# Optimization experiments

Hardware: AMD Instinct MI355X
Metric: run time of the kernel (lower is better)

The kernel has to match this reference:

```python
import jax, jax.numpy as jnp
import numpy as np

NEG_SLOPE = 0.2


def gat_conv(x, edge_index, W, a_src, a_dst, b):
    # PyG GATConv (heads=1, add_self_loops=True, concat -> out_channels)
    N = x.shape[0]
    h = x @ W                                   # [N, F_out]
    loops = jnp.arange(N, dtype=edge_index.dtype)
    src = jnp.concatenate([edge_index[0], loops])   # message sources (x_j)
    dst = jnp.concatenate([edge_index[1], loops])   # message targets (x_i)
    # attention logits: e = LeakyReLU(a_src . h_j + a_dst . h_i)
    alpha_s = h @ a_src                          # [N]
    alpha_d = h @ a_dst                          # [N]
    e = jax.nn.leaky_relu(alpha_s[src] + alpha_d[dst], NEG_SLOPE)  # [E+N]
    # segment softmax over incoming edges of each dst node
    m = jax.ops.segment_max(e, dst, num_segments=N)
    e = jnp.exp(e - m[dst])
    denom = jax.ops.segment_sum(e, dst, num_segments=N)
    alpha = e / denom[dst]                       # self-loops guarantee denom > 0
    # weighted scatter-sum aggregation
    out = jax.ops.segment_sum(alpha[:, None] * h[src], dst, num_segments=N)
    return out + b


def setup_inputs() -> dict:
    key = jax.random.key(0)
    ks = jax.random.split(key, 10)
    N, E, F_in, H, F_out = 100000, 3200000, 54, 16, 16
    x = jax.random.normal(ks[0], (N, F_in), dtype=jnp.float32)
    edge_index = jax.random.randint(ks[1], (2, E), 0, N, dtype=jnp.int64)
    s1 = 1.0 / np.sqrt(F_in)
    s2 = 1.0 / np.sqrt(H)
    return {
        "x": x,
        "edge_index": edge_index,
        "W1": jax.random.uniform(ks[2], (F_in, H), jnp.float32, -s1, s1),
        "a1_src": jax.random.uniform(ks[3], (H,), jnp.float32, -s2, s2),
        "a1_dst": jax.random.uniform(ks[4], (H,), jnp.float32, -s2, s2),
        "b1": jnp.zeros((H,), jnp.float32),
        "W2": jax.random.uniform(ks[5], (H, F_out), jnp.float32, -s2, s2),
        "a2_src": jax.random.uniform(ks[6], (F_out,), jnp.float32, -0.25, 0.25),
        "a2_dst": jax.random.uniform(ks[7], (F_out,), jnp.float32, -0.25, 0.25),
        "b2": jnp.zeros((F_out,), jnp.float32),
    }


def reference(x, edge_index, W1, a1_src, a1_dst, b1, W2, a2_src, a2_dst, b2):
    h = gat_conv(x, edge_index, W1, a1_src, a1_dst, b1)
    h = jax.nn.elu(h)
    # dropout p=0.5 is identity in eval mode
    out = gat_conv(h, edge_index, W2, a2_src, a2_dst, b2)
    return out
```

## Files before the change

kernel.cpp:

```cpp
#include <hip/hip_runtime.h>
#include <hip/hip_bf16.h>

typedef __hip_bfloat16 bf16;

static constexpr int N_NODES = 100000;
static constexpr int N_EDGES = 3200000;
static constexpr int F_IN    = 54;
static constexpr int F_HID   = 16;

static constexpr int BSHIFT    = 7;
static constexpr int BNODES    = 128;
static constexpr int NBUCK     = (N_NODES + BNODES - 1) / BNODES;
static constexpr int CAP_B     = 5120;
static constexpr int BIN_CHUNK = 8192;
static constexpr int GRDB      = (N_EDGES + BIN_CHUNK - 1) / BIN_CHUNK;
static constexpr int GRDN_F    = (N_NODES + 1023) / 1024;

static constexpr size_t WS_FLAGS  = 0;
static constexpr size_t WS_ADST   = 4;
static constexpr size_t WS_ADST2  = 100004;
static constexpr size_t WS_BCNT   = 200004;
static constexpr size_t WS_ROWBEG = 201028;
static constexpr size_t WS_ROWCNT = 301028;
static constexpr size_t WS_HC1    = 401028;
static constexpr size_t WS_HC2    = 2001028;
static constexpr size_t WS_BEDGES = 3601028;
static constexpr size_t WS_SRCS   = 7604868;
static constexpr size_t WS_BUCKET_END = WS_SRCS + (size_t)NBUCK * CAP_B;
static constexpr size_t WS_FB_DEN     = 3601028;
static constexpr size_t WS_FB_AS      = 3701028;
static constexpr size_t WS_ATOMIC_END = 3801028;

__device__ __forceinline__ float lrelu(float v) { return fmaxf(v, 0.2f * v); }
__device__ __forceinline__ float loadf(const void* p, int i, bool f32) {
    return f32 ? ((const float*)p)[i] : __bfloat162float(((const bf16*)p)[i]);
}
__device__ __forceinline__ unsigned f2bf(float f) {
    unsigned u = __float_as_uint(f);
    return (u + 0x7FFFu + ((u >> 16) & 1u)) >> 16;
}

__global__ __launch_bounds__(256) void k_probe0(
    const void* __restrict__ x, const void* __restrict__ ei,
    int* __restrict__ flags, int* __restrict__ bcnt)
{
    __shared__ int cnt, nz;
    const int t = threadIdx.x;
    if (t == 0) { cnt = 0; nz = 0; }
    __syncthreads();
    const unsigned u = ((const unsigned*)x)[t];
    if ((u & 0x7FFFu) >= 0x4800u) atomicAdd(&cnt, 1);
    if (t < 64) {
        if (((const unsigned*)ei)[2 * t + 1] != 0u) atomicAdd(&nz, 1);
    }
    for (int i = t; i < 1024; i += 256) bcnt[i] = 0;
    __syncthreads();
    if (t == 0) flags[0] = ((cnt >= 16) ? 1 : 0) | ((nz == 0) ? 2 : 0);
}

__global__ __launch_bounds__(1024, 8) void k_binfeat(
    const void* __restrict__ ei, const void* __restrict__ x,
    const void* __restrict__ W1, const void* __restrict__ a_s,
    const void* __restrict__ a_d, const int* __restrict__ flags,
    int* __restrict__ bcnt, int* __restrict__ bedges,
    unsigned* __restrict__ hc, float* __restrict__ adst)
{
    __shared__ int            hist[NBUCK];
    __shared__ int            base[NBUCK];
    __shared__ int            cval[BIN_CHUNK];
    __shared__ unsigned short cbkt[BIN_CHUNK];
    __shared__ float Wl[F_IN * F_HID];
    __shared__ float asl[F_HID];
    __shared__ float adl[F_HID];
    const int t = threadIdx.x;
    const bool f32 = flags[0] & 1;
    const bool i64 = flags[0] & 2;

    if (blockIdx.x < GRDB) {
        const int e0 = blockIdx.x * BIN_CHUNK;
        const int valid = min(BIN_CHUNK, N_EDGES - e0);
        for (int i = t; i < NBUCK; i += 1024) hist[i] = 0;
        __syncthreads();
#pragma unroll
        for (int i = 0; i < BIN_CHUNK / 1024; ++i) {
            const int idx = i * 1024 + t;
            const int e = e0 + idx;
            if (idx < valid) {
                int s, d;
                if (i64) {
                    s = ((const int*)ei)[2 * (size_t)e];
                    d = ((const int*)ei)[2 * ((size_t)N_EDGES + e)];
                } else {
                    s = ((const int*)ei)[e];
                    d = ((const int*)ei)[(size_t)N_EDGES + e];
                }
                const int b = d >> BSHIFT;
                cval[idx] = (s << BSHIFT) | (d & (BNODES - 1));
                cbkt[idx] = (unsigned short)b;
                atomicAdd(&hist[b], 1);
            }
        }
        __syncthreads();
        for (int i = t; i < NBUCK; i += 1024) {
            const int c = hist[i];
            base[i] = c ? atomicAdd(&bcnt[i], c) : 0;
            hist[i] = 0;
        }
        __syncthreads();
#pragma unroll
        for (int i = 0; i < BIN_CHUNK / 1024; ++i) {
            const int idx = i * 1024 + t;
            if (idx < valid) {
                const int b = cbkt[idx];
                const int r = atomicAdd(&hist[b], 1);
                const int pos = base[b] + r;
                if (pos < CAP_B) bedges[(size_t)b * CAP_B + pos] = cval[idx];
            }
        }
    } else {
        for (int i = t; i < F_IN * F_HID; i += 1024) Wl[i] = loadf(W1, i, f32);
        if (t < F_HID) { asl[t] = loadf(a_s, t, f32); adl[t] = loadf(a_d, t, f32); }
        __syncthreads();
        const int node = (blockIdx.x - GRDB) * 1024 + t;
        if (node >= N_NODES) return;

        float h[F_HID];
#pragma unroll
        for (int k = 0; k < F_HID; ++k) h[k] = 0.f;
        if (f32) {
            const float2* xp = (const float2*)((const float*)x + (size_t)node * F_IN);
#pragma unroll
            for (int j = 0; j < F_IN / 2; ++j) {
                const float2 v = xp[j];
#pragma unroll
                for (int k = 0; k < F_HID; ++k) {
                    h[k] = fmaf(v.x, Wl[(2*j)   * F_HID + k], h[k]);
                    h[k] = fmaf(v.y, Wl[(2*j+1) * F_HID + k], h[k]);
                }
            }
        } else {
            const unsigned* xu = (const unsigned*)x + (size_t)node * (F_IN / 2);
#pragma unroll
            for (int j = 0; j < F_IN / 2; ++j) {
                const unsigned u = xu[j];
                const float v0 = __uint_as_float(u << 16);
                const float v1 = __uint_as_float(u & 0xFFFF0000u);
#pragma unroll
                for (int k = 0; k < F_HID; ++k) {
                    h[k] = fmaf(v0, Wl[(2*j)   * F_HID + k], h[k]);
                    h[k] = fmaf(v1, Wl[(2*j+1) * F_HID + k], h[k]);
                }
            }
        }
        float s = 0.f, d = 0.f;
#pragma unroll
        for (int k = 0; k < F_HID; ++k) { s = fmaf(h[k], asl[k], s); d = fmaf(h[k], adl[k], d); }
        adst[node] = d;
        const unsigned ab = f2bf(s) << 16;
        unsigned pk[F_HID];
#pragma unroll
        for (int k = 0; k < F_HID; ++k) pk[k] = f2bf(h[k]) | ab;
        uint4* hb = (uint4*)(hc + (size_t)node * F_HID);
#pragma unroll
        for (int q = 0; q < 4; ++q)
            hb[q] = make_uint4(pk[4*q], pk[4*q+1], pk[4*q+2], pk[4*q+3]);
    }
}

__global__ __launch_bounds__(512) void k_bsort(
    const int* __restrict__ bcnt, const int* __restrict__ bedges,
    int* __restrict__ rowbeg, int* __restrict__ rowcnt, int* __restrict__ srcs)
{
    __shared__ int hist[BNODES];
    __shared__ int scan[BNODES];
    __shared__ int cur[BNODES];
    const int t = threadIdx.x;
    const int b = blockIdx.x;
    const int n0 = b << BSHIFT;
    if (t < BNODES) hist[t] = 0;
    __syncthreads();
    const int cnt = min(bcnt[b], CAP_B);
    const int* be = bedges + (size_t)b * CAP_B;
    for (int e = t; e < cnt; e += 512)
        atomicAdd(&hist[be[e] & (BNODES - 1)], 1);
    __syncthreads();
    if (t < BNODES) scan[t] = (hist[t] + 3) & ~3;
    __syncthreads();
#pragma unroll
    for (int off = 1; off < BNODES; off <<= 1) {
        const int v = (t < BNODES && t >= off) ? scan[t - off] : 0;
        __syncthreads();
        if (t < BNODES) scan[t] += v;
        __syncthreads();
    }
    if (t < BNODES) {
        const int ex = scan[t] - ((hist[t] + 3) & ~3);
        cur[t] = ex;
        const int node = n0 + t;
        if (node < N_NODES) {
            rowbeg[node] = b * CAP_B + ex;
            rowcnt[node] = hist[t];
        }
    }
    __syncthreads();
    for (int e = t; e < cnt; e += 512) {
        const int p = be[e];
        const int dl = p & (BNODES - 1);
        const int r = atomicAdd(&cur[dl], 1);
        if (r < CAP_B) srcs[(size_t)b * CAP_B + r] = p >> BSHIFT;
    }
}

__global__ __launch_bounds__(256) void k_agg1(
    const int* __restrict__ rowbeg, const int* __restrict__ rowcnt,
    const int* __restrict__ srcs, const float* __restrict__ adst,
    const unsigned* __restrict__ hc, const void* __restrict__ b1,
    const void* __restrict__ W2, const void* __restrict__ a_s2,
    const void* __restrict__ a_d2, const int* __restrict__ flags,
    unsigned* __restrict__ hc2, float* __restrict__ adst2)
{
    __shared__ float Wl[F_HID * F_HID];
    __shared__ float asl[F_HID];
    __shared__ float adl[F_HID];
    __shared__ float bl[F_HID];
    const bool f32 = flags[0] & 1;
    const int t = threadIdx.x;
    if (t < F_HID * F_HID) Wl[t] = loadf(W2, t, f32);
    if (t < F_HID) {
        asl[t] = loadf(a_s2, t, f32);
        adl[t] = loadf(a_d2, t, f32);
        bl[t]  = loadf(b1, t, f32);
    }
    __syncthreads();

    const int k = t & 15;
    const int node = blockIdx.x * 16 + (t >> 4);
    const float adn = adst[node];
    const unsigned vs = hc[(size_t)node * F_HID + k];
    const float w0 = __expf(lrelu(__uint_as_float(vs & 0xFFFF0000u) + adn));
    float denom = w0;
    float acc = w0 * __uint_as_float(vs << 16);
    const int n = rowcnt[node];
    const int* sp = srcs + rowbeg[node];
    int i = 0;
    if (n >= 8) {
        int4 sa = *(const int4*)(sp);
        int4 sb = *(const int4*)(sp + 4);
        while (true) {
            const bool more = (i + 16 <= n);
            int4 na, nb;
            if (more) {
                na = *(const int4*)(sp + i + 8);
                nb = *(const int4*)(sp + i + 12);
            }
            const unsigned v0 = hc[(size_t)sa.x * F_HID + k];
            const unsigned v1 = hc[(size_t)sa.y * F_HID + k];
            const unsigned v2 = hc[(size_t)sa.z * F_HID + k];
            const unsigned v3 = hc[(size_t)sa.w * F_HID + k];
            const unsigned v4 = hc[(size_t)sb.x * F_HID + k];
            const unsigned v5 = hc[(size_t)sb.y * F_HID + k];
            const unsigned v6 = hc[(size_t)sb.z * F_HID + k];
            const unsigned v7 = hc[(size_t)sb.w * F_HID + k];
            const float e0 = __expf(lrelu(__uint_as_float(v0 & 0xFFFF0000u) + adn));
            const float e1 = __expf(lrelu(__uint_as_float(v1 & 0xFFFF0000u) + adn));
            const float e2 = __expf(lrelu(__uint_as_float(v2 & 0xFFFF0000u) + adn));
            const float e3 = __expf(lrelu(__uint_as_float(v3 & 0xFFFF0000u) + adn));
            const float e4 = __expf(lrelu(__uint_as_float(v4 & 0xFFFF0000u) + adn));
            const float e5 = __expf(lrelu(__uint_as_float(v5 & 0xFFFF0000u) + adn));
            const float e6 = __expf(lrelu(__uint_as_float(v6 & 0xFFFF0000u) + adn));
            const float e7 = __expf(lrelu(__uint_as_float(v7 & 0xFFFF0000u) + adn));
            denom += (e0 + e1 + e2 + e3) + (e4 + e5 + e6 + e7);
            acc = fmaf(e0, __uint_as_float(v0 << 16), acc);
            acc = fmaf(e1, __uint_as_float(v1 << 16), acc);
            acc = fmaf(e2, __uint_as_float(v2 << 16), acc);
            acc = fmaf(e3, __uint_as_float(v3 << 16), acc);
            acc = fmaf(e4, __uint_as_float(v4 << 16), acc);
            acc = fmaf(e5, __uint_as_float(v5 << 16), acc);
            acc = fmaf(e6, __uint_as_float(v6 << 16), acc);
            acc = fmaf(e7, __uint_as_float(v7 << 16), acc);
            i += 8;
            if (!more) break;
            sa = na; sb = nb;
        }
    }
    if (i + 4 <= n) {
        const int4 sa = *(const int4*)(sp + i);
        const unsigned v0 = hc[(size_t)sa.x * F_HID + k];
        const unsigned v1 = hc[(size_t)sa.y * F_HID + k];
        const unsigned v2 = hc[(size_t)sa.z * F_HID + k];
        const unsigned v3 = hc[(size_t)sa.w * F_HID + k];
        const float e0 = __expf(lrelu(__uint_as_float(v0 & 0xFFFF0000u) + adn));
        const float e1 = __expf(lrelu(__uint_as_float(v1 & 0xFFFF0000u) + adn));
        const float e2 = __expf(lrelu(__uint_as_float(v2 & 0xFFFF0000u) + adn));
        const float e3 = __expf(lrelu(__uint_as_float(v3 & 0xFFFF0000u) + adn));
        denom += (e0 + e1) + (e2 + e3);
        acc = fmaf(e0, __uint_as_float(v0 << 16), acc);
        acc = fmaf(e1, __uint_as_float(v1 << 16), acc);
        acc = fmaf(e2, __uint_as_float(v2 << 16), acc);
        acc = fmaf(e3, __uint_as_float(v3 << 16), acc);
        i += 4;
    }
    for (; i < n; ++i) {
        const unsigned v = hc[(size_t)sp[i] * F_HID + k];
        const float w = __expf(lrelu(__uint_as_float(v & 0xFFFF0000u) + adn));
        denom += w;
        acc = fmaf(w, __uint_as_float(v << 16), acc);
    }
    float z = acc / denom + bl[k];
    z = z > 0.f ? z : expm1f(z);

    float hh = 0.f;
#pragma unroll
    for (int j = 0; j < F_HID; ++j) {
        const float zj = __shfl(z, j, 16);
        hh = fmaf(zj, Wl[j * F_HID + k], hh);
    }
    float s2 = hh * asl[k], d2 = hh * adl[k];
#pragma unroll
    for (int off = 1; off < 16; off <<= 1) {
        s2 += __shfl_xor(s2, off, 16);
        d2 += __shfl_xor(d2, off, 16);
    }
    hc2[(size_t)node * F_HID + k] = f2bf(hh) | (f2bf(s2) << 16);
    if (k == 0) adst2[node] = d2;
}

__global__ __launch_bounds__(256) void k_agg2(
    const int* __restrict__ rowbeg, const int* __restrict__ rowcnt,
    const int* __restrict__ srcs, const float* __restrict__ adst,
    const unsigned* __restrict__ hc, const void* __restrict__ b2,
    const int* __restrict__ flags, float* __restrict__ outp)
{
    const bool f32 = flags[0] & 1;
    const int t = threadIdx.x;
    const int k = t & 15;
    const int node = blockIdx.x * 16 + (t >> 4);
    const float adn = adst[node];
    const unsigned vs = hc[(size_t)node * F_HID + k];
    const float w0 = __expf(lrelu(__uint_as_float(vs & 0xFFFF0000u) + adn));
    float denom = w0;
    float acc = w0 * __uint_as_float(vs << 16);
    const int n = rowcnt[node];
    const int* sp = srcs + rowbeg[node];
    int i = 0;
    if (n >= 8) {
        int4 sa = *(const int4*)(sp);
        int4 sb = *(const int4*)(sp + 4);
        while (true) {
            const bool more = (i + 16 <= n);
            int4 na, nb;
            if (more) {
                na = *(const int4*)(sp + i + 8);
                nb = *(const int4*)(sp + i + 12);
            }
            const unsigned v0 = hc[(size_t)sa.x * F_HID + k];
            const unsigned v1 = hc[(size_t)sa.y * F_HID + k];
            const unsigned v2 = hc[(size_t)sa.z * F_HID + k];
            const unsigned v3 = hc[(size_t)sa.w * F_HID + k];
            const unsigned v4 = hc[(size_t)sb.x * F_HID + k];
            const unsigned v5 = hc[(size_t)sb.y * F_HID + k];
            const unsigned v6 = hc[(size_t)sb.z * F_HID + k];
            const unsigned v7 = hc[(size_t)sb.w * F_HID + k];
            const float e0 = __expf(lrelu(__uint_as_float(v0 & 0xFFFF0000u) + adn));
            const float e1 = __expf(lrelu(__uint_as_float(v1 & 0xFFFF0000u) + adn));
            const float e2 = __expf(lrelu(__uint_as_float(v2 & 0xFFFF0000u) + adn));
            const float e3 = __expf(lrelu(__uint_as_float(v3 & 0xFFFF0000u) + adn));
            const float e4 = __expf(lrelu(__uint_as_float(v4 & 0xFFFF0000u) + adn));
            const float e5 = __expf(lrelu(__uint_as_float(v5 & 0xFFFF0000u) + adn));
            const float e6 = __expf(lrelu(__uint_as_float(v6 & 0xFFFF0000u) + adn));
            const float e7 = __expf(lrelu(__uint_as_float(v7 & 0xFFFF0000u) + adn));
            denom += (e0 + e1 + e2 + e3) + (e4 + e5 + e6 + e7);
            acc = fmaf(e0, __uint_as_float(v0 << 16), acc);
            acc = fmaf(e1, __uint_as_float(v1 << 16), acc);
            acc = fmaf(e2, __uint_as_float(v2 << 16), acc);
            acc = fmaf(e3, __uint_as_float(v3 << 16), acc);
            acc = fmaf(e4, __uint_as_float(v4 << 16), acc);
            acc = fmaf(e5, __uint_as_float(v5 << 16), acc);
            acc = fmaf(e6, __uint_as_float(v6 << 16), acc);
            acc = fmaf(e7, __uint_as_float(v7 << 16), acc);
            i += 8;
            if (!more) break;
            sa = na; sb = nb;
        }
    }
    if (i + 4 <= n) {
        const int4 sa = *(const int4*)(sp + i);
        const unsigned v0 = hc[(size_t)sa.x * F_HID + k];
        const unsigned v1 = hc[(size_t)sa.y * F_HID + k];
        const unsigned v2 = hc[(size_t)sa.z * F_HID + k];
        const unsigned v3 = hc[(size_t)sa.w * F_HID + k];
        const float e0 = __expf(lrelu(__uint_as_float(v0 & 0xFFFF0000u) + adn));
        const float e1 = __expf(lrelu(__uint_as_float(v1 & 0xFFFF0000u) + adn));
        const float e2 = __expf(lrelu(__uint_as_float(v2 & 0xFFFF0000u) + adn));
        const float e3 = __expf(lrelu(__uint_as_float(v3 & 0xFFFF0000u) + adn));
        denom += (e0 + e1) + (e2 + e3);
        acc = fmaf(e0, __uint_as_float(v0 << 16), acc);
        acc = fmaf(e1, __uint_as_float(v1 << 16), acc);
        acc = fmaf(e2, __uint_as_float(v2 << 16), acc);
        acc = fmaf(e3, __uint_as_float(v3 << 16), acc);
        i += 4;
    }
    for (; i < n; ++i) {
        const unsigned v = hc[(size_t)sp[i] * F_HID + k];
        const float w = __expf(lrelu(__uint_as_float(v & 0xFFFF0000u) + adn));
        denom += w;
        acc = fmaf(w, __uint_as_float(v << 16), acc);
    }
    outp[(size_t)node * F_HID + k] = acc / denom + loadf(b2, k, f32);
}

__global__ __launch_bounds__(256) void k_feat1(
    const void* __restrict__ x, const void* __restrict__ W1,
    const void* __restrict__ a_s, const void* __restrict__ a_d,
    const int* __restrict__ flags,
    float* __restrict__ hbuf, float* __restrict__ asrc, float* __restrict__ adst)
{
    const bool f32 = flags[0] & 1;
    __shared__ float Wl[F_IN * F_HID];
    __shared__ float asl[F_HID];
    __shared__ float adl[F_HID];
    const int t = threadIdx.x;
    for (int i = t; i < F_IN * F_HID; i += 256) Wl[i] = loadf(W1, i, f32);
    if (t < F_HID) { asl[t] = loadf(a_s, t, f32); adl[t] = loadf(a_d, t, f32); }
    __syncthreads();
    const int node = blockIdx.x * 256 + t;
    if (node >= N_NODES) return;
    float h[F_HID];
#pragma unroll
    for (int k = 0; k < F_HID; ++k) h[k] = 0.f;
    if (f32) {
        const float2* xp = (const float2*)((const float*)x + (size_t)node * F_IN);
#pragma unroll
        for (int j = 0; j < F_IN / 2; ++j) {
            const float2 v = xp[j];
#pragma unroll
            for (int k = 0; k < F_HID; ++k) {
                h[k] = fmaf(v.x, Wl[(2*j)   * F_HID + k], h[k]);
                h[k] = fmaf(v.y, Wl[(2*j+1) * F_HID + k], h[k]);
            }
        }
    } else {
        const unsigned* xu = (const unsigned*)x + (size_t)node * (F_IN / 2);
#pragma unroll
        for (int j = 0; j < F_IN / 2; ++j) {
            const unsigned u = xu[j];
            const float v0 = __uint_as_float(u << 16);
            const float v1 = __uint_as_float(u & 0xFFFF0000u);
#pragma unroll
            for (int k = 0; k < F_HID; ++k) {
                h[k] = fmaf(v0, Wl[(2*j)   * F_HID + k], h[k]);
                h[k] = fmaf(v1, Wl[(2*j+1) * F_HID + k], h[k]);
            }
        }
    }
    float s = 0.f, d = 0.f;
#pragma unroll
    for (int k = 0; k < F_HID; ++k) { s = fmaf(h[k], asl[k], s); d = fmaf(h[k], adl[k], d); }
    asrc[node] = s; adst[node] = d;
    float4* hb = (float4*)(hbuf + (size_t)node * F_HID);
#pragma unroll
    for (int q = 0; q < 4; ++q)
        hb[q] = make_float4(h[4*q], h[4*q+1], h[4*q+2], h[4*q+3]);
}

__global__ __launch_bounds__(256) void k_selfinit(
    const float* __restrict__ asrc, const float* __restrict__ adst,
    const float* __restrict__ h, float* __restrict__ denom, float* __restrict__ acc)
{
    const int t = blockIdx.x * 256 + threadIdx.x;
    if (t >= N_NODES * F_HID) return;
    const int n = t >> 4;
    const float w0 = __expf(lrelu(asrc[n] + adst[n]));
    if ((t & 15) == 0) denom[n] = w0;
    acc[t] = w0 * h[t];
}

__global__ __launch_bounds__(256) void k_edge(
    const void* __restrict__ ei, const int* __restrict__ flags,
    const float* __restrict__ asrc, const float* __restrict__ adst,
    const float* __restrict__ hbuf,
    float* __restrict__ denom, float* __restrict__ acc)
{
    const int e = blockIdx.x * 256 + threadIdx.x;
    if (e >= N_EDGES) return;
    int s, d;
    if (flags[0] & 2) {
        const long long* e64 = (const long long*)ei;
        s = (int)e64[e]; d = (int)e64[(size_t)N_EDGES + e];
    } else {
        const int* e32 = (const int*)ei;
        s = e32[e]; d = e32[(size_t)N_EDGES + e];
    }
    const float w = __expf(lrelu(asrc[s] + adst[d]));
    atomicAdd(&denom[d], w);
    const float4* hs = (const float4*)(hbuf + (size_t)s * F_HID);
    float* ad = acc + (size_t)d * F_HID;
#pragma unroll
    for (int q = 0; q < 4; ++q) {
        const float4 hv = hs[q];
        atomicAdd(ad + 4*q + 0, w * hv.x);
        atomicAdd(ad + 4*q + 1, w * hv.y);
        atomicAdd(ad + 4*q + 2, w * hv.z);
        atomicAdd(ad + 4*q + 3, w * hv.w);
    }
}

__global__ __launch_bounds__(256) void k_div_elu(
    float* __restrict__ acc, const float* __restrict__ denom,
    const void* __restrict__ b1, const int* __restrict__ flags)
{
    const bool f32 = flags[0] & 1;
    const int t = blockIdx.x * 256 + threadIdx.x;
    if (t >= N_NODES * F_HID) return;
    const float v = acc[t] / denom[t >> 4] + loadf(b1, t & 15, f32);
    acc[t] = v > 0.f ? v : expm1f(v);
}

__global__ __launch_bounds__(256) void k_mid(
    const float* __restrict__ z,
    const void* __restrict__ W2, const void* __restrict__ a_s2,
    const void* __restrict__ a_d2, const int* __restrict__ flags,
    float* __restrict__ h2, float* __restrict__ asrc, float* __restrict__ adst)
{
    const bool f32 = flags[0] & 1;
    __shared__ float Wl[F_HID * F_HID];
    __shared__ float asl[F_HID];
    __shared__ float adl[F_HID];
    const int t = threadIdx.x;
    if (t < F_HID * F_HID) Wl[t] = loadf(W2, t, f32);
    if (t < F_HID) { asl[t] = loadf(a_s2, t, f32); adl[t] = loadf(a_d2, t, f32); }
    __syncthreads();
    const int node = blockIdx.x * 256 + t;
    if (node >= N_NODES) return;
    float zr[F_HID];
    const float4* zi = (const float4*)(z + (size_t)node * F_HID);
#pragma unroll
    for (int q = 0; q < 4; ++q) {
        const float4 zv = zi[q];
        zr[4*q+0]=zv.x; zr[4*q+1]=zv.y; zr[4*q+2]=zv.z; zr[4*q+3]=zv.w;
    }
    float h[F_HID];
#pragma unroll
    for (int k = 0; k < F_HID; ++k) h[k] = 0.f;
#pragma unroll
    for (int j = 0; j < F_HID; ++j) {
        const float zv = zr[j];
#pragma unroll
        for (int k = 0; k < F_HID; ++k) h[k] = fmaf(zv, Wl[j * F_HID + k], h[k]);
    }
    float s = 0.f, d = 0.f;
#pragma unroll
    for (int k = 0; k < F_HID; ++k) { s = fmaf(h[k], asl[k], s); d = fmaf(h[k], adl[k], d); }
    asrc[node] = s; adst[node] = d;
    float4* hb = (float4*)(h2 + (size_t)node * F_HID);
#pragma unroll
    for (int q = 0; q < 4; ++q)
        hb[q] = make_float4(h[4*q], h[4*q+1], h[4*q+2], h[4*q+3]);
}

__global__ __launch_bounds__(256) void k_out(
    const float* __restrict__ acc, const float* __restrict__ denom,
    const void* __restrict__ b2, const int* __restrict__ flags,
    float* __restrict__ out)
{
    const bool f32 = flags[0] & 1;
    const int t = blockIdx.x * 256 + threadIdx.x;
    if (t >= N_NODES * F_HID) return;
    out[t] = acc[t] / denom[t >> 4] + loadf(b2, t & 15, f32);
}

__global__ __launch_bounds__(256) void k_diag(float* __restrict__ out, float v)
{
    const int t = blockIdx.x * 256 + threadIdx.x;
    if (t < N_NODES * F_HID) out[t] = v;
}

extern "C" void kernel_launch(void* const* d_in, const int* in_sizes, int n_in,
                              void* d_out, int out_size, void* d_ws, size_t ws_size,
                              hipStream_t stream) {
    const void* x   = d_in[0];
    const void* ei  = d_in[1];
    const void* W1  = d_in[2];
    const void* a1s = d_in[3];
    const void* a1d = d_in[4];
    const void* b1  = d_in[5];
    const void* W2  = d_in[6];
    const void* a2s = d_in[7];
    const void* a2d = d_in[8];
    const void* b2  = d_in[9];
    float* out = (float*)d_out;

    float* ws = (float*)d_ws;
    int*      flags  = (int*)(ws + WS_FLAGS);
    float*    adst   = ws + WS_ADST;
    float*    adst2  = ws + WS_ADST2;
    int*      bcnt   = (int*)(ws + WS_BCNT);
    int*      rowbeg = (int*)(ws + WS_ROWBEG);
    int*      rowcnt = (int*)(ws + WS_ROWCNT);
    unsigned* hc1    = (unsigned*)(ws + WS_HC1);
    unsigned* hc2    = (unsigned*)(ws + WS_HC2);
    int*      bedges = (int*)(ws + WS_BEDGES);
    int*      srcs   = (int*)(ws + WS_SRCS);

    const dim3 blk(256);
    const dim3 grdN((N_NODES + 255) / 256);
    const dim3 grdE((N_EDGES + 255) / 256);
    const dim3 grdO((N_NODES * F_HID + 255) / 256);
    const dim3 grdBF(GRDB + GRDN_F);
    const dim3 grdS(NBUCK);
    const dim3 grdA(N_NODES / 16);

    if (ws_size >= WS_BUCKET_END * 4) {
        k_probe0 <<<dim3(1), blk, 0, stream>>>(x, ei, flags, bcnt);
        k_binfeat<<<grdBF, dim3(1024), 0, stream>>>(ei, x, W1, a1s, a1d, flags,
                                                    bcnt, bedges, hc1, adst);
        k_bsort  <<<grdS, dim3(512), 0, stream>>>(bcnt, bedges, rowbeg, rowcnt, srcs);
        k_agg1   <<<grdA, blk, 0, stream>>>(rowbeg, rowcnt, srcs, adst, hc1,
                                            b1, W2, a2s, a2d, flags, hc2, adst2);
        k_agg2   <<<grdA, blk, 0, stream>>>(rowbeg, rowcnt, srcs, adst2, hc2,
                                            b2, flags, out);
    } else if (ws_size >= WS_ATOMIC_END * 4) {
        float* fb_h   = ws + WS_HC1;
        float* fb_acc = ws + WS_HC2;
        float* fb_den = ws + WS_FB_DEN;
        float* fb_as  = ws + WS_FB_AS;
        float* fb_ad  = ws + WS_ADST;
        k_probe0 <<<dim3(1), blk, 0, stream>>>(x, ei, flags, bcnt);
        k_feat1  <<<grdN, blk, 0, stream>>>(x, W1, a1s, a1d, flags, fb_h, fb_as, fb_ad);
        k_selfinit<<<grdO, blk, 0, stream>>>(fb_as, fb_ad, fb_h, fb_den, fb_acc);
        k_edge   <<<grdE, blk, 0, stream>>>(ei, flags, fb_as, fb_ad, fb_h, fb_den, fb_acc);
        k_div_elu<<<grdO, blk, 0, stream>>>(fb_acc, fb_den, b1, flags);
        k_mid    <<<grdN, blk, 0, stream>>>(fb_acc, W2, a2s, a2d, flags, fb_h, fb_as, fb_ad);
        k_selfinit<<<grdO, blk, 0, stream>>>(fb_as, fb_ad, fb_h, fb_den, fb_acc);
        k_edge   <<<grdE, blk, 0, stream>>>(ei, flags, fb_as, fb_ad, fb_h, fb_den, fb_acc);
        k_out    <<<grdO, blk, 0, stream>>>(fb_acc, fb_den, b2, flags, out);
    } else {
        k_diag<<<grdO, blk, 0, stream>>>(out, (float)(ws_size >> 10));
    }
}
```

Baseline: 258.2 us.

## Drop per-node CSR sort; aggregate bucketed edges with LDS atomics

Removes the k_bsort kernel that built per-node CSR rows from 128-node buckets. Both aggregation kernels now run one 512-thread block per bucket and stream the unsorted bucket edges directly, accumulating softmax numerators and denominators into shared-memory arrays with atomics. This saves a kernel launch plus the global write and read of the sorted source array. In exchange it adds LDS atomic contention and loses the per-node register accumulation, and the summation order becomes nondeterministic.

After: 880.2 us. +241.0%, slower.

```diff
diff --git a/kernel.cpp b/kernel.cpp
--- a/kernel.cpp
+++ b/kernel.cpp
@@ -167,246 +167,193 @@
     }
 }
 
-__global__ __launch_bounds__(512) void k_bsort(
+__global__ __launch_bounds__(512, 4) void k_agg1(
     const int* __restrict__ bcnt, const int* __restrict__ bedges,
-    int* __restrict__ rowbeg, int* __restrict__ rowcnt, int* __restrict__ srcs)
-{
-    __shared__ int hist[BNODES];
-    __shared__ int scan[BNODES];
-    __shared__ int cur[BNODES];
+    const float* __restrict__ adst, const unsigned* __restrict__ hc,
+    const void* __restrict__ b1, const void* __restrict__ W2,
+    const void* __restrict__ a_s2, const void* __restrict__ a_d2,
+    const int* __restrict__ flags,
+    unsigned* __restrict__ hc2, float* __restrict__ adst2)
+{
+    __shared__ float Wl[F_HID * F_HID];
+    __shared__ float asl[F_HID], adl[F_HID], bl[F_HID];
+    __shared__ float adL[BNODES];
+    __shared__ float accL[BNODES * 17];
+    __shared__ float denL[BNODES];
+    const bool f32 = flags[0] & 1;
     const int t = threadIdx.x;
     const int b = blockIdx.x;
     const int n0 = b << BSHIFT;
-    if (t < BNODES) hist[t] = 0;
-    __syncthreads();
-    const int cnt = min(bcnt[b], CAP_B);
-    const int* be = bedges + (size_t)b * CAP_B;
-    for (int e = t; e < cnt; e += 512)
-        atomicAdd(&hist[be[e] & (BNODES - 1)], 1);
-    __syncthreads();
-    if (t < BNODES) scan[t] = (hist[t] + 3) & ~3;
-    __syncthreads();
-#pragma unroll
-    for (int off = 1; off < BNODES; off <<= 1) {
-        const int v = (t < BNODES && t >= off) ? scan[t - off] : 0;
-        __syncthreads();
-        if (t < BNODES) scan[t] += v;
-        __syncthreads();
-    }
-    if (t < BNODES) {
-        const int ex = scan[t] - ((hist[t] + 3) & ~3);
-        cur[t] = ex;
-        const int node = n0 + t;
-        if (node < N_NODES) {
-            rowbeg[node] = b * CAP_B + ex;
-            rowcnt[node] = hist[t];
-        }
-    }
-    __syncthreads();
-    for (int e = t; e < cnt; e += 512) {
-        const int p = be[e];
-        const int dl = p & (BNODES - 1);
-        const int r = atomicAdd(&cur[dl], 1);
-        if (r < CAP_B) srcs[(size_t)b * CAP_B + r] = p >> BSHIFT;
-    }
-}
-
-__global__ __launch_bounds__(256) void k_agg1(
-    const int* __restrict__ rowbeg, const int* __restrict__ rowcnt,
-    const int* __restrict__ srcs, const float* __restrict__ adst,
-    const unsigned* __restrict__ hc, const void* __restrict__ b1,
-    const void* __restrict__ W2, const void* __restrict__ a_s2,
-    const void* __restrict__ a_d2, const int* __restrict__ flags,
-    unsigned* __restrict__ hc2, float* __restrict__ adst2)
-{
-    __shared__ float Wl[F_HID * F_HID];
-    __shared__ float asl[F_HID];
-    __shared__ float adl[F_HID];
-    __shared__ float bl[F_HID];
-    const bool f32 = flags[0] & 1;
-    const int t = threadIdx.x;
     if (t < F_HID * F_HID) Wl[t] = loadf(W2, t, f32);
     if (t < F_HID) {
         asl[t] = loadf(a_s2, t, f32);
         adl[t] = loadf(a_d2, t, f32);
         bl[t]  = loadf(b1, t, f32);
     }
-    __syncthreads();
-
-    const int k = t & 15;
-    const int node = blockIdx.x * 16 + (t >> 4);
-    const float adn = adst[node];
-    const unsigned vs = hc[(size_t)node * F_HID + k];
-    const float w0 = __expf(lrelu(__uint_as_float(vs & 0xFFFF0000u) + adn));
-    float denom = w0;
-    float acc = w0 * __uint_as_float(vs << 16);
-    const int n = rowcnt[node];
-    const int* sp = srcs + rowbeg[node];
-    int i = 0;
-    if (n >= 8) {
-        int4 sa = *(const int4*)(sp);
-        int4 sb = *(const int4*)(sp + 4);
-        while (true) {
-            const bool more = (i + 16 <= n);
-            int4 na, nb;
-            if (more) {
-                na = *(const int4*)(sp + i + 8);
-                nb = *(const int4*)(sp + i + 12);
-            }
-            const unsigned v0 = hc[(size_t)sa.x * F_HID + k];
-            const unsigned v1 = hc[(size_t)sa.y * F_HID + k];
-            const unsigned v2 = hc[(size_t)sa.z * F_HID + k];
-            const unsigned v3 = hc[(size_t)sa.w * F_HID + k];
-            const unsigned v4 = hc[(size_t)sb.x * F_HID + k];
-            const unsigned v5 = hc[(size_t)sb.y * F_HID + k];
-            const unsigned v6 = hc[(size_t)sb.z * F_HID + k];
-            const unsigned v7 = hc[(size_t)sb.w * F_HID + k];
-            const float e0 = __expf(lrelu(__uint_as_float(v0 & 0xFFFF0000u) + adn));
-            const float e1 = __expf(lrelu(__uint_as_float(v1 & 0xFFFF0000u) + adn));
-            const float e2 = __expf(lrelu(__uint_as_float(v2 & 0xFFFF0000u) + adn));
-            const float e3 = __expf(lrelu(__uint_as_float(v3 & 0xFFFF0000u) + adn));
-            const float e4 = __expf(lrelu(__uint_as_float(v4 & 0xFFFF0000u) + adn));
-            const float e5 = __expf(lrelu(__uint_as_float(v5 & 0xFFFF0000u) + adn));
-            const float e6 = __expf(lrelu(__uint_as_float(v6 & 0xFFFF0000u) + adn));
-            const float e7 = __expf(lrelu(__uint_as_float(v7 & 0xFFFF0000u) + adn));
-            denom += (e0 + e1 + e2 + e3) + (e4 + e5 + e6 + e7);
-            acc = fmaf(e0, __uint_as_float(v0 << 16), acc);
-            acc = fmaf(e1, __uint_as_float(v1 << 16), acc);
-            acc = fmaf(e2, __uint_as_float(v2 << 16), acc);
-            acc = fmaf(e3, __uint_as_float(v3 << 16), acc);
-            acc = fmaf(e4, __uint_as_float(v4 << 16), acc);
-            acc = fmaf(e5, __uint_as_float(v5 << 16), acc);
-            acc = fmaf(e6, __uint_as_float(v6 << 16), acc);
-            acc = fmaf(e7, __uint_as_float(v7 << 16), acc);
-            i += 8;
-            if (!more) break;
-            sa = na; sb = nb;
-        }
-    }
-    if (i + 4 <= n) {
-        const int4 sa = *(const int4*)(sp + i);
-        const unsigned v0 = hc[(size_t)sa.x * F_HID + k];
-        const unsigned v1 = hc[(size_t)sa.y * F_HID + k];
-        const unsigned v2 = hc[(size_t)sa.z * F_HID + k];
-        const unsigned v3 = hc[(size_t)sa.w * F_HID + k];
-        const float e0 = __expf(lrelu(__uint_as_float(v0 & 0xFFFF0000u) + adn));
-        const float e1 = __expf(lrelu(__uint_as_float(v1 & 0xFFFF0000u) + adn));
-        const float e2 = __expf(lrelu(__uint_as_float(v2 & 0xFFFF0000u) + adn));
-        const float e3 = __expf(lrelu(__uint_as_float(v3 & 0xFFFF0000u) + adn));
-        denom += (e0 + e1) + (e2 + e3);
-        acc = fmaf(e0, __uint_as_float(v0 << 16), acc);
-        acc = fmaf(e1, __uint_as_float(v1 << 16), acc);
-        acc = fmaf(e2, __uint_as_float(v2 << 16), acc);
-        acc = fmaf(e3, __uint_as_float(v3 << 16), acc);
-        i += 4;
-    }
-    for (; i < n; ++i) {
-        const unsigned v = hc[(size_t)sp[i] * F_HID + k];
-        const float w = __expf(lrelu(__uint_as_float(v & 0xFFFF0000u) + adn));
-        denom += w;
-        acc = fmaf(w, __uint_as_float(v << 16), acc);
-    }
-    float z = acc / denom + bl[k];
-    z = z > 0.f ? z : expm1f(z);
-
-    float hh = 0.f;
-#pragma unroll
-    for (int j = 0; j < F_HID; ++j) {
-        const float zj = __shfl(z, j, 16);
-        hh = fmaf(zj, Wl[j * F_HID + k], hh);
-    }
-    float s2 = hh * asl[k], d2 = hh * adl[k];
-#pragma unroll
-    for (int off = 1; off < 16; off <<= 1) {
-        s2 += __shfl_xor(s2, off, 16);
-        d2 += __shfl_xor(d2, off, 16);
-    }
-    hc2[(size_t)node * F_HID + k] = f2bf(hh) | (f2bf(s2) << 16);
-    if (k == 0) adst2[node] = d2;
-}
-
-__global__ __launch_bounds__(256) void k_agg2(
-    const int* __restrict__ rowbeg, const int* __restrict__ rowcnt,
-    const int* __restrict__ srcs, const float* __restrict__ adst,
-    const unsigned* __restrict__ hc, const void* __restrict__ b2,
-    const int* __restrict__ flags, float* __restrict__ outp)
-{
+    if (t < BNODES) {
+        const int node = n0 + t;
+        adL[t] = (node < N_NODES) ? adst[node] : 0.f;
+    }
+    __syncthreads();
+
+    const int k    = t & 15;
+    const int slot = t >> 4;
+#pragma unroll
+    for (int it = 0; it < 4; ++it) {
+        const int dl = it * 32 + slot;
+        const int node = n0 + dl;
+        if (node < N_NODES) {
+            const unsigned vs = hc[((size_t)node << 4) + k];
+            const float w0 = __expf(lrelu(__uint_as_float(vs & 0xFFFF0000u) + adL[dl]));
+            accL[dl * 17 + k] = w0 * __uint_as_float(vs << 16);
+            if (k == 0) denL[dl] = w0;
+        } else {
+            accL[dl * 17 + k] = 0.f;
+            if (k == 0) denL[dl] = 1.f;
+        }
+    }
+    __syncthreads();
+
+    const int cnt = min(bcnt[b], CAP_B);
+    const int* cv = bedges + (size_t)b * CAP_B;
+    int e = slot;
+    for (; e + 96 < cnt; e += 128) {
+        const int p0 = cv[e], p1 = cv[e + 32], p2 = cv[e + 64], p3 = cv[e + 96];
+        const int d0 = p0 & 127, d1 = p1 & 127, d2 = p2 & 127, d3 = p3 & 127;
+        const unsigned v0 = hc[((size_t)(p0 >> 7) << 4) + k];
+        const unsigned v1 = hc[((size_t)(p1 >> 7) << 4) + k];
+        const unsigned v2 = hc[((size_t)(p2 >> 7) << 4) + k];
+        const unsigned v3 = hc[((size_t)(p3 >> 7) << 4) + k];
+        const float w0 = __expf(lrelu(__uint_as_float(v0 & 0xFFFF0000u) + adL[d0]));
+        const float w1 = __expf(lrelu(__uint_as_float(v1 & 0xFFFF0000u) + adL[d1]));
+        const float w2 = __expf(lrelu(__uint_as_float(v2 & 0xFFFF0000u) + adL[d2]));
+        const float w3 = __expf(lrelu(__uint_as_float(v3 & 0xFFFF0000u) + adL[d3]));
+        atomicAdd(&accL[d0 * 17 + k], w0 * __uint_as_float(v0 << 16));
+        atomicAdd(&accL[d1 * 17 + k], w1 * __uint_as_float(v1 << 16));
+        atomicAdd(&accL[d2 * 17 + k], w2 * __uint_as_float(v2 << 16));
+        atomicAdd(&accL[d3 * 17 + k], w3 * __uint_as_float(v3 << 16));
+        if (k == 0) {
+            atomicAdd(&denL[d0], w0);
+            atomicAdd(&denL[d1], w1);
+            atomicAdd(&denL[d2], w2);
+            atomicAdd(&denL[d3], w3);
+        }
+    }
+    for (; e < cnt; e += 32) {
+        const int p = cv[e];
+        const int dl = p & 127;
+        const unsigned v = hc[((size_t)(p >> 7) << 4) + k];
+        const float w = __expf(lrelu(__uint_as_float(v & 0xFFFF0000u) + adL[dl]));
+        atomicAdd(&accL[dl * 17 + k], w * __uint_as_float(v << 16));
+        if (k == 0) atomicAdd(&denL[dl], w);
+    }
+    __syncthreads();
+
+#pragma unroll
+    for (int it = 0; it < 4; ++it) {
+        const int dl = it * 32 + slot;
+        const int node = n0 + dl;
+        if (node >= N_NODES) continue;
+        float z = accL[dl * 17 + k] / denL[dl] + bl[k];
+        z = z > 0.f ? z : expm1f(z);
+        float hh = 0.f;
+#pragma unroll
+        for (int j = 0; j < F_HID; ++j) {
+            const float zj = __shfl(z, j, 16);
+            hh = fmaf(zj, Wl[j * F_HID + k], hh);
+        }
+        float s2 = hh * asl[k], d2v = hh * adl[k];
+#pragma unroll
+        for (int off = 1; off < 16; off <<= 1) {
+            s2  += __shfl_xor(s2, off, 16);
+            d2v += __shfl_xor(d2v, off, 16);
+        }
+        hc2[((size_t)node << 4) + k] = f2bf(hh) | (f2bf(s2) << 16);
+        if (k == 0) adst2[node] = d2v;
+    }
+}
+
+__global__ __launch_bounds__(512, 4) void k_agg2(
+    const int* __restrict__ bcnt, const int* __restrict__ bedges,
+    const float* __restrict__ adst, const unsigned* __restrict__ hc,
+    const void* __restrict__ b2, const int* __restrict__ flags,
+    float* __restrict__ outp)
+{
+    __shared__ float bl[F_HID];
+    __shared__ float adL[BNODES];
+    __shared__ float accL[BNODES * 17];
+    __shared__ float denL[BNODES];
     const bool f32 = flags[0] & 1;
     const int t = threadIdx.x;
-    const int k = t & 15;
-    const int node = blockIdx.x * 16 + (t >> 4);
-    const float adn = adst[node];
-    const unsigned vs = hc[(size_t)node * F_HID + k];
-    const float w0 = __expf(lrelu(__uint_as_float(vs & 0xFFFF0000u) + adn));
-    float denom = w0;
-    float acc = w0 * __uint_as_float(vs << 16);
-    const int n = rowcnt[node];
-    const int* sp = srcs + rowbeg[node];
-    int i = 0;
-    if (n >= 8) {
-        int4 sa = *(const int4*)(sp);
-        int4 sb = *(const int4*)(sp + 4);
-        while (true) {
-            const bool more = (i + 16 <= n);
-            int4 na, nb;
-            if (more) {
-                na = *(const int4*)(sp + i + 8);
-                nb = *(const int4*)(sp + i + 12);
-            }
-            const unsigned v0 = hc[(size_t)sa.x * F_HID + k];
-            const unsigned v1 = hc[(size_t)sa.y * F_HID + k];
-            const unsigned v2 = hc[(size_t)sa.z * F_HID + k];
-            const unsigned v3 = hc[(size_t)sa.w * F_HID + k];
-            const unsigned v4 = hc[(size_t)sb.x * F_HID + k];
-            const unsigned v5 = hc[(size_t)sb.y * F_HID + k];
-            const unsigned v6 = hc[(size_t)sb.z * F_HID + k];
-            const unsigned v7 = hc[(size_t)sb.w * F_HID + k];
-            const float e0 = __expf(lrelu(__uint_as_float(v0 & 0xFFFF0000u) + adn));
-            const float e1 = __expf(lrelu(__uint_as_float(v1 & 0xFFFF0000u) + adn));
-            const float e2 = __expf(lrelu(__uint_as_float(v2 & 0xFFFF0000u) + adn));
-            const float e3 = __expf(lrelu(__uint_as_float(v3 & 0xFFFF0000u) + adn));
-            const float e4 = __expf(lrelu(__uint_as_float(v4 & 0xFFFF0000u) + adn));
-            const float e5 = __expf(lrelu(__uint_as_float(v5 & 0xFFFF0000u) + adn));
-            const float e6 = __expf(lrelu(__uint_as_float(v6 & 0xFFFF0000u) + adn));
-            const float e7 = __expf(lrelu(__uint_as_float(v7 & 0xFFFF0000u) + adn));
-            denom += (e0 + e1 + e2 + e3) + (e4 + e5 + e6 + e7);
-            acc = fmaf(e0, __uint_as_float(v0 << 16), acc);
-            acc = fmaf(e1, __uint_as_float(v1 << 16), acc);
-            acc = fmaf(e2, __uint_as_float(v2 << 16), acc);
-            acc = fmaf(e3, __uint_as_float(v3 << 16), acc);
-            acc = fmaf(e4, __uint_as_float(v4 << 16), acc);
-            acc = fmaf(e5, __uint_as_float(v5 << 16), acc);
-            acc = fmaf(e6, __uint_as_float(v6 << 16), acc);
-            acc = fmaf(e7, __uint_as_float(v7 << 16), acc);
-            i += 8;
-            if (!more) break;
-            sa = na; sb = nb;
-        }
-    }
-    if (i + 4 <= n) {
-        const int4 sa = *(const int4*)(sp + i);
-        const unsigned v0 = hc[(size_t)sa.x * F_HID + k];
-        const unsigned v1 = hc[(size_t)sa.y * F_HID + k];
-        const unsigned v2 = hc[(size_t)sa.z * F_HID + k];
-        const unsigned v3 = hc[(size_t)sa.w * F_HID + k];
-        const float e0 = __expf(lrelu(__uint_as_float(v0 & 0xFFFF0000u) + adn));
-        const float e1 = __expf(lrelu(__uint_as_float(v1 & 0xFFFF0000u) + adn));
-        const float e2 = __expf(lrelu(__uint_as_float(v2 & 0xFFFF0000u) + adn));
-        const float e3 = __expf(lrelu(__uint_as_float(v3 & 0xFFFF0000u) + adn));
-        denom += (e0 + e1) + (e2 + e3);
-        acc = fmaf(e0, __uint_as_float(v0 << 16), acc);
-        acc = fmaf(e1, __uint_as_float(v1 << 16), acc);
-        acc = fmaf(e2, __uint_as_float(v2 << 16), acc);
-        acc = fmaf(e3, __uint_as_float(v3 << 16), acc);
-        i += 4;
-    }
-    for (; i < n; ++i) {
-        const unsigned v = hc[(size_t)sp[i] * F_HID + k];
-        const float w = __expf(lrelu(__uint_as_float(v & 0xFFFF0000u) + adn));
-        denom += w;
-        acc = fmaf(w, __uint_as_float(v << 16), acc);
-    }
-    outp[(size_t)node * F_HID + k] = acc / denom + loadf(b2, k, f32);
+    const int b = blockIdx.x;
+    const int n0 = b << BSHIFT;
+    if (t < F_HID) bl[t] = loadf(b2, t, f32);
+    if (t < BNODES) {
+        const int node = n0 + t;
+        adL[t] = (node < N_NODES) ? adst[node] : 0.f;
+    }
+    __syncthreads();
+
+    const int k    = t & 15;
+    const int slot = t >> 4;
+#pragma unroll
+    for (int it = 0; it < 4; ++it) {
+        const int dl = it * 32 + slot;
+        const int node = n0 + dl;
+        if (node < N_NODES) {
+            const unsigned vs = hc[((size_t)node << 4) + k];
+            const float w0 = __expf(lrelu(__uint_as_float(vs & 0xFFFF0000u) + adL[dl]));
+            accL[dl * 17 + k] = w0 * __uint_as_float(vs << 16);
+            if (k == 0) denL[dl] = w0;
+        } else {
+            accL[dl * 17 + k] = 0.f;
+            if (k == 0) denL[dl] = 1.f;
+        }
+    }
+    __syncthreads();
+
+    const int cnt = min(bcnt[b], CAP_B);
+    const int* cv = bedges + (size_t)b * CAP_B;
+    int e = slot;
+    for (; e + 96 < cnt; e += 128) {
+        const int p0 = cv[e], p1 = cv[e + 32], p2 = cv[e + 64], p3 = cv[e + 96];
+        const int d0 = p0 & 127, d1 = p1 & 127, d2 = p2 & 127, d3 = p3 & 127;
+        const unsigned v0 = hc[((size_t)(p0 >> 7) << 4) + k];
+        const unsigned v1 = hc[((size_t)(p1 >> 7) << 4) + k];
+        const unsigned v2 = hc[((size_t)(p2 >> 7) << 4) + k];
+        const unsigned v3 = hc[((size_t)(p3 >> 7) << 4) + k];
+        const float w0 = __expf(lrelu(__uint_as_float(v0 & 0xFFFF0000u) + adL[d0]));
+        const float w1 = __expf(lrelu(__uint_as_float(v1 & 0xFFFF0000u) + adL[d1]));
+        const float w2 = __expf(lrelu(__uint_as_float(v2 & 0xFFFF0000u) + adL[d2]));
+        const float w3 = __expf(lrelu(__uint_as_float(v3 & 0xFFFF0000u) + adL[d3]));
+        atomicAdd(&accL[d0 * 17 + k], w0 * __uint_as_float(v0 << 16));
+        atomicAdd(&accL[d1 * 17 + k], w1 * __uint_as_float(v1 << 16));
+        atomicAdd(&accL[d2 * 17 + k], w2 * __uint_as_float(v2 << 16));
+        atomicAdd(&accL[d3 * 17 + k], w3 * __uint_as_float(v3 << 16));
+        if (k == 0) {
+            atomicAdd(&denL[d0], w0);
+            atomicAdd(&denL[d1], w1);
+            atomicAdd(&denL[d2], w2);
+            atomicAdd(&denL[d3], w3);
+        }
+    }
+    for (; e < cnt; e += 32) {
+        const int p = cv[e];
+        const int dl = p & 127;
+        const unsigned v = hc[((size_t)(p >> 7) << 4) + k];
+        const float w = __expf(lrelu(__uint_as_float(v & 0xFFFF0000u) + adL[dl]));
+        atomicAdd(&accL[dl * 17 + k], w * __uint_as_float(v << 16));
+        if (k == 0) atomicAdd(&denL[dl], w);
+    }
+    __syncthreads();
+
+#pragma unroll
+    for (int it = 0; it < 4; ++it) {
+        const int dl = it * 32 + slot;
+        const int node = n0 + dl;
+        if (node >= N_NODES) continue;
+        outp[((size_t)node << 4) + k] = accL[dl * 17 + k] / denL[dl] + bl[k];
+    }
 }
 
 __global__ __launch_bounds__(256) void k_feat1(
@@ -595,30 +542,25 @@
     float*    adst   = ws + WS_ADST;
     float*    adst2  = ws + WS_ADST2;
     int*      bcnt   = (int*)(ws + WS_BCNT);
-    int*      rowbeg = (int*)(ws + WS_ROWBEG);
-    int*      rowcnt = (int*)(ws + WS_ROWCNT);
     unsigned* hc1    = (unsigned*)(ws + WS_HC1);
     unsigned* hc2    = (unsigned*)(ws + WS_HC2);
     int*      bedges = (int*)(ws + WS_BEDGES);
-    int*      srcs   = (int*)(ws + WS_SRCS);
 
     const dim3 blk(256);
     const dim3 grdN((N_NODES + 255) / 256);
     const dim3 grdE((N_EDGES + 255) / 256);
     const dim3 grdO((N_NODES * F_HID + 255) / 256);
     const dim3 grdBF(GRDB + GRDN_F);
-    const dim3 grdS(NBUCK);
-    const dim3 grdA(N_NODES / 16);
+    const dim3 grdB(NBUCK);
 
     if (ws_size >= WS_BUCKET_END * 4) {
         k_probe0 <<<dim3(1), blk, 0, stream>>>(x, ei, flags, bcnt);
         k_binfeat<<<grdBF, dim3(1024), 0, stream>>>(ei, x, W1, a1s, a1d, flags,
                                                     bcnt, bedges, hc1, adst);
-        k_bsort  <<<grdS, dim3(512), 0, stream>>>(bcnt, bedges, rowbeg, rowcnt, srcs);
-        k_agg1   <<<grdA, blk, 0, stream>>>(rowbeg, rowcnt, srcs, adst, hc1,
-                                            b1, W2, a2s, a2d, flags, hc2, adst2);
-        k_agg2   <<<grdA, blk, 0, stream>>>(rowbeg, rowcnt, srcs, adst2, hc2,
-                                            b2, flags, out);
+        k_agg1   <<<grdB, dim3(512), 0, stream>>>(bcnt, bedges, adst, hc1,
+                                                  b1, W2, a2s, a2d, flags, hc2, adst2);
+        k_agg2   <<<grdB, dim3(512), 0, stream>>>(bcnt, bedges, adst2, hc2,
+                                                  b2, flags, out);
     } else if (ws_size >= WS_ATOMIC_END * 4) {
         float* fb_h   = ws + WS_HC1;
         float* fb_acc = ws + WS_HC2;
```
